# Kernel optimization log

Measured on AMD Instinct MI355X. Metric: run time of the kernel, lower is better.

## Reference

```python
import jax, jax.numpy as jnp
import numpy as np

N_NODES = 50000
N_EDGES = 300000
NODE_DIM = 11
EDGE_DIM = 5
HID = 256
L = 4
G = 1024  # num graphs
BN_EPS = 1e-5


def setup_inputs() -> dict:
    key = jax.random.key(0)
    ks = jax.random.split(key, 24)
    s = 0.05
    inp = {
        "x": jax.random.normal(ks[0], (N_NODES, NODE_DIM), jnp.float32),
        "edge_index": jax.random.randint(ks[1], (2, N_EDGES), 0, N_NODES, jnp.int32),
        "edge_attr": jax.random.normal(ks[2], (N_EDGES, EDGE_DIM), jnp.float32),
        "batch": jnp.sort(jax.random.randint(ks[3], (N_NODES,), 0, G, jnp.int32)),
        # node encoder
        "enc_W": jax.random.normal(ks[4], (NODE_DIM, HID), jnp.float32) * s,
        "enc_b": jnp.zeros((HID,), jnp.float32),
        # per-layer GINE params (stacked over layers)
        "edge_W": jax.random.normal(ks[5], (L, EDGE_DIM, HID), jnp.float32) * s,
        "edge_b": jnp.zeros((L, HID), jnp.float32),
        "mlp_W1": jax.random.normal(ks[6], (L, HID, HID), jnp.float32) * s,
        "mlp_b1": jnp.zeros((L, HID), jnp.float32),
        "mlp_W2": jax.random.normal(ks[7], (L, HID, HID), jnp.float32) * s,
        "mlp_b2": jnp.zeros((L, HID), jnp.float32),
        "bn_g": jnp.ones((L, HID), jnp.float32),
        "bn_b": jnp.zeros((L, HID), jnp.float32),
        # head: 3*HID -> HID -> HID//2 -> 1
        "head_W1": jax.random.normal(ks[8], (3 * HID, HID), jnp.float32) * s,
        "head_b1": jnp.zeros((HID,), jnp.float32),
        "head_W2": jax.random.normal(ks[9], (HID, HID // 2), jnp.float32) * s,
        "head_b2": jnp.zeros((HID // 2,), jnp.float32),
        "head_W3": jax.random.normal(ks[10], (HID // 2, 1), jnp.float32) * s,
        "head_b3": jnp.zeros((1,), jnp.float32),
    }
    return inp


def _forward(x, edge_attr, enc_W, enc_b, edge_W, edge_b, mlp_W1, mlp_b1,
             mlp_W2, mlp_b2, bn_g, bn_b, head_W1, head_b1, head_W2, head_b2,
             head_W3, head_b3, edge_index, batch):
    n = x.shape[0]
    src, dst = edge_index[0], edge_index[1]  # messages flow src(j) -> dst(i)
    h = jax.nn.relu(x @ enc_W + enc_b)  # [N, HID]
    for l in range(L):
        e = edge_attr @ edge_W[l] + edge_b[l]                 # [E, HID]
        msg = jax.nn.relu(h[src] + e)                         # [E, HID]
        aggr = jax.ops.segment_sum(msg, dst, num_segments=n)  # [N, HID]
        z = h + aggr                                          # (1+eps)*h + aggr, eps=0
        z = jax.nn.relu(z @ mlp_W1[l] + mlp_b1[l]) @ mlp_W2[l] + mlp_b2[l]
        # BatchNorm over node dim (batch statistics)
        mu = jnp.mean(z, axis=0)
        var = jnp.var(z, axis=0)
        z = (z - mu) * jax.lax.rsqrt(var + BN_EPS) * bn_g[l] + bn_b[l]
        h = jax.nn.relu(z) + h  # residual
    # mean / add / max pooling per graph
    sums = jax.ops.segment_sum(h, batch, num_segments=G)      # [G, HID]
    cnt = jax.ops.segment_sum(jnp.ones((n, 1), h.dtype), batch, num_segments=G)
    mean = sums / jnp.maximum(cnt, 1.0)
    mx = jax.ops.segment_max(h, batch, num_segments=G)
    g = jnp.concatenate([mean, sums, mx], axis=1)             # [G, 3*HID]
    g = jax.nn.relu(g @ head_W1 + head_b1)
    g = jax.nn.relu(g @ head_W2 + head_b2)
    out = g @ head_W3 + head_b3
    return out.reshape(-1)  # [G]


def reference(x, edge_index, edge_attr, batch, enc_W, enc_b, edge_W, edge_b,
              mlp_W1, mlp_b1, mlp_W2, mlp_b2, bn_g, bn_b, head_W1, head_b1,
              head_W2, head_b2, head_W3, head_b3):
    return _forward(x, edge_attr, enc_W, enc_b, edge_W, edge_b, mlp_W1, mlp_b1,
                    mlp_W2, mlp_b2, bn_g, bn_b, head_W1, head_b1, head_W2,
                    head_b2, head_W3, head_b3, edge_index, batch)
```

## Files before the change

### kernel.cpp

```cpp
#include <hip/hip_runtime.h>

#define N_NODES 50000
#define N_EDGES 300000
#define G_GRAPHS 1024
#define HID 256
#define NLAYERS 4
#define PAD_SLOTS (N_EDGES + 3 * N_NODES + 64)
#define BMT 224

typedef unsigned short ushort_t;
typedef __attribute__((ext_vector_type(8))) short bf16x8;
typedef __attribute__((ext_vector_type(8))) unsigned short u16x8;
typedef __attribute__((ext_vector_type(4))) float f32x4;

__device__ __forceinline__ float bf2f(ushort_t u) {
  unsigned int x = ((unsigned int)u) << 16;
  return __builtin_bit_cast(float, x);
}
__device__ __forceinline__ ushort_t f2bf(float f) {
  unsigned int x = __builtin_bit_cast(unsigned int, f);
  unsigned int lsb = (x >> 16) & 1u;
  x += 0x7fffu + lsb;
  return (ushort_t)(x >> 16);
}

__global__ __launch_bounds__(256) void k_encoder(const float* __restrict__ x,
    const float* __restrict__ W, const float* __restrict__ b,
    ushort_t* __restrict__ h, int n)
{
  int j = threadIdx.x;
  float wcol[11];
#pragma unroll
  for (int k = 0; k < 11; ++k) wcol[k] = W[k * HID + j];
  float bj = b[j];
  __shared__ float xs[8][11];
  int base = blockIdx.x * 8;
  if (j < 88) {
    int r = j / 11, k = j % 11;
    int row = base + r;
    if (row < n) xs[r][k] = x[row * 11 + k];
  }
  __syncthreads();
#pragma unroll
  for (int r = 0; r < 8; ++r) {
    int row = base + r;
    if (row >= n) break;
    float acc = bj;
#pragma unroll
    for (int k = 0; k < 11; ++k) acc += xs[r][k] * wcol[k];
    h[(size_t)row * HID + j] = f2bf(fmaxf(acc, 0.f));
  }
}

__global__ __launch_bounds__(256) void k_hist(const int* __restrict__ dst,
    int* __restrict__ offs, int E)
{
  int e = blockIdx.x * 256 + threadIdx.x;
  if (e < E) atomicAdd(&offs[dst[e]], 1);
}

__global__ __launch_bounds__(1024) void k_scanA(int* __restrict__ offs,
    int* __restrict__ btot, int n)
{
  __shared__ int wsum[16];
  int tid = threadIdx.x, lane = tid & 63, wid = tid >> 6;
  int idx = blockIdx.x * 1024 + tid;
  int cnt = (idx < n) ? offs[idx] : 0;
  int v = (cnt + 3) & ~3;
  int x = v;
#pragma unroll
  for (int off = 1; off < 64; off <<= 1) {
    int t = __shfl_up(x, off);
    if (lane >= off) x += t;
  }
  if (lane == 63) wsum[wid] = x;
  __syncthreads();
  if (wid == 0 && lane < 16) {
    int w = wsum[lane];
#pragma unroll
    for (int off = 1; off < 16; off <<= 1) {
      int t = __shfl_up(w, off);
      if (lane >= off) w += t;
    }
    wsum[lane] = w;
  }
  __syncthreads();
  int wbase = (wid == 0) ? 0 : wsum[wid - 1];
  if (idx < n) offs[idx] = wbase + x - v;
  if (tid == 0) btot[blockIdx.x] = wsum[15];
}

__global__ __launch_bounds__(1024) void k_scanC(int* __restrict__ offs,
    int* __restrict__ pstart, const int* __restrict__ btot, int n)
{
  __shared__ int sbase;
  if (threadIdx.x == 0) {
    int s = 0;
    for (int i = 0; i < (int)blockIdx.x; ++i) s += btot[i];
    sbase = s;
    if (blockIdx.x == gridDim.x - 1) pstart[n] = s + btot[blockIdx.x];
  }
  __syncthreads();
  int idx = blockIdx.x * 1024 + threadIdx.x;
  if (idx < n) {
    int v = offs[idx] + sbase;
    offs[idx] = v;
    pstart[idx] = v;
  }
}

__global__ __launch_bounds__(256) void k_fill(const int* __restrict__ src,
    const int* __restrict__ dst, int* __restrict__ offs,
    int* __restrict__ esrc, ushort_t* __restrict__ eab,
    const float* __restrict__ ea, int E)
{
  int e = blockIdx.x * 256 + threadIdx.x;
  if (e < E) {
    int d = dst[e];
    int p = atomicAdd(&offs[d], 1);
    esrc[p] = src[e];
    const float* ep = ea + (size_t)e * 5;
    ushort4 lo = make_ushort4(f2bf(ep[0]), f2bf(ep[1]), f2bf(ep[2]), f2bf(ep[3]));
    ushort4 hi = make_ushort4(f2bf(ep[4]), (ushort_t)0x3f80u, 0, 0);
    *(ushort4*)&eab[(size_t)p * 8] = lo;
    *(ushort4*)&eab[(size_t)p * 8 + 4] = hi;
  }
}

__global__ __launch_bounds__(256) void k_prep(const float* __restrict__ W1,
    const float* __restrict__ W2, ushort_t* __restrict__ Wt1,
    ushort_t* __restrict__ Wt2)
{
  __shared__ float ld[16][257];
  int mat = blockIdx.y & (NLAYERS - 1);
  int which = blockIdx.y >> 2;
  const float* Wm = (which ? W2 : W1) + (size_t)mat * HID * HID;
  ushort_t* Wtm = (which ? Wt2 : Wt1) + (size_t)mat * HID * HID;
  int k0 = blockIdx.x * 16;
  int tid = threadIdx.x;
#pragma unroll
  for (int i = 0; i < 16; ++i) ld[i][tid] = Wm[(size_t)(k0 + i) * HID + tid];
  __syncthreads();
#pragma unroll
  for (int v = 0; v < 4; ++v) {
    ushort4 u = make_ushort4(f2bf(ld[v*4+0][tid]), f2bf(ld[v*4+1][tid]),
                             f2bf(ld[v*4+2][tid]), f2bf(ld[v*4+3][tid]));
    *(ushort4*)&Wtm[(size_t)tid * HID + k0 + v * 4] = u;
  }
}

__global__ __launch_bounds__(256) void k_prept(const float* __restrict__ W,
    ushort_t* __restrict__ Wt, int K, int N)
{
  int idx = blockIdx.x * 256 + threadIdx.x;
  if (idx >= K * N) return;
  int n = idx / K, k = idx % K;
  Wt[idx] = f2bf(W[(size_t)k * N + n]);
}

__device__ __forceinline__ void edge_step(bf16x8 ev, ushort4 hv,
    const float4& w0, const float4& w1, const float4& w2, const float4& w3,
    const float4& w4, const float4& bi,
    float& ax, float& ay, float& az, float& aw)
{
  float v0 = bf2f((ushort_t)ev[0]), v1 = bf2f((ushort_t)ev[1]),
        v2 = bf2f((ushort_t)ev[2]), v3 = bf2f((ushort_t)ev[3]),
        v4 = bf2f((ushort_t)ev[4]), fl = bf2f((ushort_t)ev[5]);
  float m0 = bi.x, m1 = bi.y, m2 = bi.z, m3 = bi.w;
  m0 = fmaf(v0, w0.x, m0); m1 = fmaf(v0, w0.y, m1);
  m2 = fmaf(v0, w0.z, m2); m3 = fmaf(v0, w0.w, m3);
  m0 = fmaf(v1, w1.x, m0); m1 = fmaf(v1, w1.y, m1);
  m2 = fmaf(v1, w1.z, m2); m3 = fmaf(v1, w1.w, m3);
  m0 = fmaf(v2, w2.x, m0); m1 = fmaf(v2, w2.y, m1);
  m2 = fmaf(v2, w2.z, m2); m3 = fmaf(v2, w2.w, m3);
  m0 = fmaf(v3, w3.x, m0); m1 = fmaf(v3, w3.y, m1);
  m2 = fmaf(v3, w3.z, m2); m3 = fmaf(v3, w3.w, m3);
  m0 = fmaf(v4, w4.x, m0); m1 = fmaf(v4, w4.y, m1);
  m2 = fmaf(v4, w4.z, m2); m3 = fmaf(v4, w4.w, m3);
  m0 += bf2f(hv.x); m1 += bf2f(hv.y); m2 += bf2f(hv.z); m3 += bf2f(hv.w);
  ax = fmaf(fl, fmaxf(m0, 0.f), ax);
  ay = fmaf(fl, fmaxf(m1, 0.f), ay);
  az = fmaf(fl, fmaxf(m2, 0.f), az);
  aw = fmaf(fl, fmaxf(m3, 0.f), aw);
}

__global__ __launch_bounds__(256) void k_gather(const ushort_t* __restrict__ h,
    const int* __restrict__ pstart, const int* __restrict__ esrc,
    const ushort_t* __restrict__ eab, const float* __restrict__ eW,
    const float* __restrict__ eb, ushort_t* __restrict__ zin,
    float* __restrict__ stats, int n)
{
  int tid = threadIdx.x;
  if (blockIdx.x == 0) { stats[tid] = 0.f; stats[HID + tid] = 0.f; }
  int wave = tid >> 6, lane = tid & 63;
  int c4 = lane * 4;
  float4 w0 = *(const float4*)&eW[0 * HID + c4];
  float4 w1 = *(const float4*)&eW[1 * HID + c4];
  float4 w2 = *(const float4*)&eW[2 * HID + c4];
  float4 w3 = *(const float4*)&eW[3 * HID + c4];
  float4 w4 = *(const float4*)&eW[4 * HID + c4];
  float4 bi = *(const float4*)&eb[c4];
  int n0 = (blockIdx.x * 4 + wave) * 4;
  if (n0 >= n) return;
  int e0 = __builtin_amdgcn_readfirstlane(pstart[n0]);
  int e1 = __builtin_amdgcn_readfirstlane(pstart[n0 + 1]);
  int e2 = __builtin_amdgcn_readfirstlane(pstart[n0 + 2]);
  int e3 = __builtin_amdgcn_readfirstlane(pstart[n0 + 3]);
  int e4 = __builtin_amdgcn_readfirstlane(pstart[n0 + 4]);
  float A[4][4];
#pragma unroll
  for (int j = 0; j < 4; ++j) {
    ushort4 hv = *(const ushort4*)&h[(size_t)(n0 + j) * HID + c4];
    A[j][0] = bf2f(hv.x); A[j][1] = bf2f(hv.y);
    A[j][2] = bf2f(hv.z); A[j][3] = bf2f(hv.w);
  }
  int p = e0, pend = e4;
  if (p < pend) {
    int sA0 = esrc[p],     sA1 = esrc[p + 1], sA2 = esrc[p + 2], sA3 = esrc[p + 3];
    int sB0 = esrc[p + 4], sB1 = esrc[p + 5], sB2 = esrc[p + 6], sB3 = esrc[p + 7];
    bf16x8 eaA0 = *(const bf16x8*)&eab[(size_t)(p + 0) * 8];
    bf16x8 eaA1 = *(const bf16x8*)&eab[(size_t)(p + 1) * 8];
    bf16x8 eaA2 = *(const bf16x8*)&eab[(size_t)(p + 2) * 8];
    bf16x8 eaA3 = *(const bf16x8*)&eab[(size_t)(p + 3) * 8];
    bf16x8 eaB0 = *(const bf16x8*)&eab[(size_t)(p + 4) * 8];
    bf16x8 eaB1 = *(const bf16x8*)&eab[(size_t)(p + 5) * 8];
    bf16x8 eaB2 = *(const bf16x8*)&eab[(size_t)(p + 6) * 8];
    bf16x8 eaB3 = *(const bf16x8*)&eab[(size_t)(p + 7) * 8];
    ushort4 hA0 = *(const ushort4*)&h[(size_t)sA0 * HID + c4];
    ushort4 hA1 = *(const ushort4*)&h[(size_t)sA1 * HID + c4];
    ushort4 hA2 = *(const ushort4*)&h[(size_t)sA2 * HID + c4];
    ushort4 hA3 = *(const ushort4*)&h[(size_t)sA3 * HID + c4];
    ushort4 hB0 = *(const ushort4*)&h[(size_t)sB0 * HID + c4];
    ushort4 hB1 = *(const ushort4*)&h[(size_t)sB1 * HID + c4];
    ushort4 hB2 = *(const ushort4*)&h[(size_t)sB2 * HID + c4];
    ushort4 hB3 = *(const ushort4*)&h[(size_t)sB3 * HID + c4];
    int sC0 = esrc[p + 8],  sC1 = esrc[p + 9],  sC2 = esrc[p + 10], sC3 = esrc[p + 11];
    int sD0 = esrc[p + 12], sD1 = esrc[p + 13], sD2 = esrc[p + 14], sD3 = esrc[p + 15];
    while (true) {
      {
        float c0 = 0.f, c1 = 0.f, c2 = 0.f, c3 = 0.f;
        edge_step(eaA0, hA0, w0, w1, w2, w3, w4, bi, c0, c1, c2, c3);
        edge_step(eaA1, hA1, w0, w1, w2, w3, w4, bi, c0, c1, c2, c3);
        edge_step(eaA2, hA2, w0, w1, w2, w3, w4, bi, c0, c1, c2, c3);
        edge_step(eaA3, hA3, w0, w1, w2, w3, w4, bi, c0, c1, c2, c3);
        if (p < e1)      { A[0][0] += c0; A[0][1] += c1; A[0][2] += c2; A[0][3] += c3; }
        else if (p < e2) { A[1][0] += c0; A[1][1] += c1; A[1][2] += c2; A[1][3] += c3; }
        else if (p < e3) { A[2][0] += c0; A[2][1] += c1; A[2][2] += c2; A[2][3] += c3; }
        else             { A[3][0] += c0; A[3][1] += c1; A[3][2] += c2; A[3][3] += c3; }
      }
      p += 4;
      if (p >= pend) break;
      eaA0 = *(const bf16x8*)&eab[(size_t)(p + 4) * 8];
      eaA1 = *(const bf16x8*)&eab[(size_t)(p + 5) * 8];
      eaA2 = *(const bf16x8*)&eab[(size_t)(p + 6) * 8];
      eaA3 = *(const bf16x8*)&eab[(size_t)(p + 7) * 8];
      hA0 = *(const ushort4*)&h[(size_t)sC0 * HID + c4];
      hA1 = *(const ushort4*)&h[(size_t)sC1 * HID + c4];
      hA2 = *(const ushort4*)&h[(size_t)sC2 * HID + c4];
      hA3 = *(const ushort4*)&h[(size_t)sC3 * HID + c4];
      sC0 = esrc[p + 12]; sC1 = esrc[p + 13]; sC2 = esrc[p + 14]; sC3 = esrc[p + 15];
      {
        float c0 = 0.f, c1 = 0.f, c2 = 0.f, c3 = 0.f;
        edge_step(eaB0, hB0, w0, w1, w2, w3, w4, bi, c0, c1, c2, c3);
        edge_step(eaB1, hB1, w0, w1, w2, w3, w4, bi, c0, c1, c2, c3);
        edge_step(eaB2, hB2, w0, w1, w2, w3, w4, bi, c0, c1, c2, c3);
        edge_step(eaB3, hB3, w0, w1, w2, w3, w4, bi, c0, c1, c2, c3);
        if (p < e1)      { A[0][0] += c0; A[0][1] += c1; A[0][2] += c2; A[0][3] += c3; }
        else if (p < e2) { A[1][0] += c0; A[1][1] += c1; A[1][2] += c2; A[1][3] += c3; }
        else if (p < e3) { A[2][0] += c0; A[2][1] += c1; A[2][2] += c2; A[2][3] += c3; }
        else             { A[3][0] += c0; A[3][1] += c1; A[3][2] += c2; A[3][3] += c3; }
      }
      p += 4;
      if (p >= pend) break;
      eaB0 = *(const bf16x8*)&eab[(size_t)(p + 4) * 8];
      eaB1 = *(const bf16x8*)&eab[(size_t)(p + 5) * 8];
      eaB2 = *(const bf16x8*)&eab[(size_t)(p + 6) * 8];
      eaB3 = *(const bf16x8*)&eab[(size_t)(p + 7) * 8];
      hB0 = *(const ushort4*)&h[(size_t)sD0 * HID + c4];
      hB1 = *(const ushort4*)&h[(size_t)sD1 * HID + c4];
      hB2 = *(const ushort4*)&h[(size_t)sD2 * HID + c4];
      hB3 = *(const ushort4*)&h[(size_t)sD3 * HID + c4];
      sD0 = esrc[p + 12]; sD1 = esrc[p + 13]; sD2 = esrc[p + 14]; sD3 = esrc[p + 15];
    }
  }
#pragma unroll
  for (int j = 0; j < 4; ++j) {
    *(ushort4*)&zin[(size_t)(n0 + j) * HID + c4] =
        make_ushort4(f2bf(A[j][0]), f2bf(A[j][1]), f2bf(A[j][2]), f2bf(A[j][3]));
  }
}

__global__ __launch_bounds__(512, 1) void k_mlp(const ushort_t* __restrict__ A,
    const ushort_t* __restrict__ Wt1, const float* __restrict__ b1,
    const ushort_t* __restrict__ Wt2, const float* __restrict__ b2,
    ushort_t* __restrict__ out, float* __restrict__ stats, int M)
{
  __shared__ alignas(16) ushort_t T[BMT][264];
  int tid = threadIdx.x;
  int wave = tid >> 6, lane = tid & 63;
  int m = lane & 15, quad = lane >> 4;
  int col0 = wave * 32;
  int row0 = blockIdx.x * BMT;

#pragma unroll
  for (int i = 0; i < 14; ++i) {
    int flat = i * 512 + tid;
    int row = flat >> 5, kc = flat & 31;
    int gr = row0 + row; if (gr > M - 1) gr = M - 1;
    u16x8 v = *(const u16x8*)(A + (size_t)gr * HID + kc * 8);
    *(u16x8*)&T[row][kc * 8] = v;
  }
  bf16x8 w1f[2][8];
#pragma unroll
  for (int nt = 0; nt < 2; ++nt)
#pragma unroll
    for (int kt = 0; kt < 8; ++kt)
      w1f[nt][kt] = *(const bf16x8*)(
          Wt1 + (size_t)(col0 + nt * 16 + m) * HID + kt * 32 + quad * 8);
  float bv1[2] = {b1[col0 + m], b1[col0 + 16 + m]};
  float bv2[2] = {b2[col0 + m], b2[col0 + 16 + m]};
  __syncthreads();

  f32x4 acc[14][2];
#pragma unroll
  for (int mt = 0; mt < 14; ++mt) {
    acc[mt][0] = (f32x4){0.f, 0.f, 0.f, 0.f};
    acc[mt][1] = (f32x4){0.f, 0.f, 0.f, 0.f};
    bf16x8 af[8];
#pragma unroll
    for (int kt = 0; kt < 8; ++kt)
      af[kt] = *(const bf16x8*)&T[mt * 16 + m][kt * 32 + quad * 8];
#pragma unroll
    for (int kt = 0; kt < 8; ++kt) {
      acc[mt][0] = __builtin_amdgcn_mfma_f32_16x16x32_bf16(af[kt], w1f[0][kt], acc[mt][0], 0, 0, 0);
      acc[mt][1] = __builtin_amdgcn_mfma_f32_16x16x32_bf16(af[kt], w1f[1][kt], acc[mt][1], 0, 0, 0);
    }
  }
  __syncthreads();

#pragma unroll
  for (int mt = 0; mt < 14; ++mt)
#pragma unroll
    for (int nt = 0; nt < 2; ++nt)
#pragma unroll
      for (int reg = 0; reg < 4; ++reg)
        T[mt * 16 + quad * 4 + reg][col0 + nt * 16 + m] =
            f2bf(fmaxf(acc[mt][nt][reg] + bv1[nt], 0.f));
  bf16x8 w2f[2][8];
#pragma unroll
  for (int nt = 0; nt < 2; ++nt)
#pragma unroll
    for (int kt = 0; kt < 8; ++kt)
      w2f[nt][kt] = *(const bf16x8*)(
          Wt2 + (size_t)(col0 + nt * 16 + m) * HID + kt * 32 + quad * 8);
  __syncthreads();

#pragma unroll
  for (int mt = 0; mt < 14; ++mt) {
    acc[mt][0] = (f32x4){0.f, 0.f, 0.f, 0.f};
    acc[mt][1] = (f32x4){0.f, 0.f, 0.f, 0.f};
    bf16x8 af[8];
#pragma unroll
    for (int kt = 0; kt < 8; ++kt)
      af[kt] = *(const bf16x8*)&T[mt * 16 + m][kt * 32 + quad * 8];
#pragma unroll
    for (int kt = 0; kt < 8; ++kt) {
      acc[mt][0] = __builtin_amdgcn_mfma_f32_16x16x32_bf16(af[kt], w2f[0][kt], acc[mt][0], 0, 0, 0);
      acc[mt][1] = __builtin_amdgcn_mfma_f32_16x16x32_bf16(af[kt], w2f[1][kt], acc[mt][1], 0, 0, 0);
    }
  }

  float csum[2] = {0.f, 0.f}, csq[2] = {0.f, 0.f};
#pragma unroll
  for (int mt = 0; mt < 14; ++mt) {
    if (row0 + mt * 16 < M) {
#pragma unroll
      for (int nt = 0; nt < 2; ++nt) {
#pragma unroll
        for (int reg = 0; reg < 4; ++reg) {
          float o = acc[mt][nt][reg] + bv2[nt];
          out[(size_t)(row0 + mt * 16 + quad * 4 + reg) * HID + col0 + nt * 16 + m] = f2bf(o);
          csum[nt] += o; csq[nt] = fmaf(o, o, csq[nt]);
        }
      }
    }
  }
#pragma unroll
  for (int nt = 0; nt < 2; ++nt) {
    float s = csum[nt], q = csq[nt];
    s += __shfl_xor(s, 16); s += __shfl_xor(s, 32);
    q += __shfl_xor(q, 16); q += __shfl_xor(q, 32);
    if (quad == 0) {
      unsafeAtomicAdd(&stats[col0 + nt * 16 + m], s);
      unsafeAtomicAdd(&stats[HID + col0 + nt * 16 + m], q);
    }
  }
}

__global__ __launch_bounds__(256) void k_bn_apply(const ushort_t* __restrict__ z,
    const float* __restrict__ stats, const float* __restrict__ g,
    const float* __restrict__ b, ushort_t* __restrict__ h, int total4)
{
  int idx = blockIdx.x * 256 + threadIdx.x;
  if (idx >= total4) return;
  int col = (idx & 63) * 4;
  const float inv_n = 1.f / (float)N_NODES;
  float sc[4], sh[4];
#pragma unroll
  for (int c = 0; c < 4; ++c) {
    float mu = stats[col + c] * inv_n;
    float var = stats[HID + col + c] * inv_n - mu * mu;
    float rs = rsqrtf(var + 1e-5f);
    sc[c] = g[col + c] * rs;
    sh[c] = b[col + c] - mu * sc[c];
  }
  ushort4 zv = *(const ushort4*)(z + (size_t)idx * 4);
  ushort4 hv = *(const ushort4*)(h + (size_t)idx * 4);
  float o0 = fmaxf(fmaf(bf2f(zv.x), sc[0], sh[0]), 0.f) + bf2f(hv.x);
  float o1 = fmaxf(fmaf(bf2f(zv.y), sc[1], sh[1]), 0.f) + bf2f(hv.y);
  float o2 = fmaxf(fmaf(bf2f(zv.z), sc[2], sh[2]), 0.f) + bf2f(hv.z);
  float o3 = fmaxf(fmaf(bf2f(zv.w), sc[3], sh[3]), 0.f) + bf2f(hv.w);
  *(ushort4*)(h + (size_t)idx * 4) = make_ushort4(f2bf(o0), f2bf(o1), f2bf(o2), f2bf(o3));
}

__device__ __forceinline__ int lbound(const int* __restrict__ b, int n, int key) {
  int lo = 0, hi = n;
  while (lo < hi) {
    int mid = (lo + hi) >> 1;
    if (b[mid] < key) lo = mid + 1; else hi = mid;
  }
  return lo;
}

__global__ __launch_bounds__(256) void k_pool_bn(const ushort_t* __restrict__ z,
    const float* __restrict__ stats, const float* __restrict__ g_,
    const float* __restrict__ b_, const ushort_t* __restrict__ h,
    const int* __restrict__ batch, ushort_t* __restrict__ gf)
{
  int g = blockIdx.x, j = threadIdx.x;
  const float inv_n = 1.f / (float)N_NODES;
  float mu = stats[j] * inv_n;
  float var = stats[HID + j] * inv_n - mu * mu;
  float rs = rsqrtf(var + 1e-5f);
  float sc = g_[j] * rs;
  float sh = b_[j] - mu * sc;
  int lo = lbound(batch, N_NODES, g);
  int hi = lbound(batch, N_NODES, g + 1);
  float s = 0.f, mx = 0.f;
  for (int i = lo; i < hi; ++i) {
    float zv = bf2f(z[(size_t)i * HID + j]);
    float hv = bf2f(h[(size_t)i * HID + j]);
    float v = fmaxf(fmaf(zv, sc, sh), 0.f) + hv;
    s += v; mx = fmaxf(mx, v);
  }
  float cntv = fmaxf((float)(hi - lo), 1.f);
  size_t base = (size_t)g * 768;
  gf[base + j] = f2bf(s / cntv);
  gf[base + 256 + j] = f2bf(s);
  gf[base + 512 + j] = f2bf(mx);
}

template<int KT, int DO_RELU>
__global__ __launch_bounds__(256, 1) void k_head_gemm(const ushort_t* __restrict__ A,
    const ushort_t* __restrict__ Bt, const float* __restrict__ bias,
    ushort_t* __restrict__ out, int M, int N)
{
  const int K = KT * 32;
  int tid = threadIdx.x;
  int wave = tid >> 6, lane = tid & 63;
  int m = lane & 15, quad = lane >> 4;
  int col = (blockIdx.y * 4 + wave) * 16 + m;
  bf16x8 bfrag[KT];
#pragma unroll
  for (int kt = 0; kt < KT; ++kt)
    bfrag[kt] = *(const bf16x8*)(Bt + (size_t)col * K + kt * 32 + quad * 8);
  float bv = bias[col];
  int ntiles = M >> 4;
  for (int t = blockIdx.x; t < ntiles; t += gridDim.x) {
    const ushort_t* Ap = A + (size_t)(t * 16 + m) * K + quad * 8;
    bf16x8 af[KT];
#pragma unroll
    for (int kt = 0; kt < KT; ++kt) af[kt] = *(const bf16x8*)(Ap + kt * 32);
    f32x4 acc = (f32x4){0.f, 0.f, 0.f, 0.f};
#pragma unroll
    for (int kt = 0; kt < KT; ++kt)
      acc = __builtin_amdgcn_mfma_f32_16x16x32_bf16(af[kt], bfrag[kt], acc, 0, 0, 0);
    int rb = t * 16 + quad * 4;
#pragma unroll
    for (int reg = 0; reg < 4; ++reg) {
      float o = acc[reg] + bv;
      if (DO_RELU) o = fmaxf(o, 0.f);
      out[(size_t)(rb + reg) * N + col] = f2bf(o);
    }
  }
}

__global__ __launch_bounds__(256) void k_head_out(const ushort_t* __restrict__ g2,
    const float* __restrict__ W3, const float* __restrict__ b3,
    float* __restrict__ out)
{
  int wave = threadIdx.x >> 6, lane = threadIdx.x & 63;
  int g = blockIdx.x * 4 + wave;
  ushort2 v = *(const ushort2*)&g2[(size_t)g * 128 + lane * 2];
  float p = bf2f(v.x) * W3[lane * 2] + bf2f(v.y) * W3[lane * 2 + 1];
#pragma unroll
  for (int off = 32; off > 0; off >>= 1) p += __shfl_down(p, off);
  if (lane == 0) out[g] = p + b3[0];
}

extern "C" void kernel_launch(void* const* d_in, const int* in_sizes, int n_in,
                              void* d_out, int out_size, void* d_ws, size_t ws_size,
                              hipStream_t stream)
{
  const float* x     = (const float*)d_in[0];
  const int*   ei    = (const int*)d_in[1];
  const float* ea    = (const float*)d_in[2];
  const int*   batch = (const int*)d_in[3];
  const float* encW  = (const float*)d_in[4];
  const float* encB  = (const float*)d_in[5];
  const float* edgeW = (const float*)d_in[6];
  const float* edgeB = (const float*)d_in[7];
  const float* W1    = (const float*)d_in[8];
  const float* b1    = (const float*)d_in[9];
  const float* W2    = (const float*)d_in[10];
  const float* b2    = (const float*)d_in[11];
  const float* bng   = (const float*)d_in[12];
  const float* bnb   = (const float*)d_in[13];
  const float* hW1   = (const float*)d_in[14];
  const float* hb1   = (const float*)d_in[15];
  const float* hW2   = (const float*)d_in[16];
  const float* hb2   = (const float*)d_in[17];
  const float* hW3   = (const float*)d_in[18];
  const float* hb3   = (const float*)d_in[19];
  float* out = (float*)d_out;

  const size_t NH = (size_t)N_NODES * HID;
  char* base = (char*)d_ws;
  auto alloc = [&](size_t bytes) -> char* {
    char* p = base; base += (bytes + 63) & ~(size_t)63; return p;
  };
  float*    stats = (float*)alloc(512 * 4);
  int*      offs  = (int*)alloc(50001 * 4);
  int*      pstart= (int*)alloc(50001 * 4);
  int*      btot  = (int*)alloc(64 * 4);
  int*      esrc  = (int*)alloc((size_t)PAD_SLOTS * 4);
  ushort_t* eab   = (ushort_t*)alloc((size_t)PAD_SLOTS * 8 * 2);
  ushort_t* Wt1   = (ushort_t*)alloc((size_t)NLAYERS * HID * HID * 2);
  ushort_t* Wt2   = (ushort_t*)alloc((size_t)NLAYERS * HID * HID * 2);
  ushort_t* hW1t  = (ushort_t*)alloc((size_t)768 * 256 * 2);
  ushort_t* hW2t  = (ushort_t*)alloc((size_t)256 * 128 * 2);
  ushort_t* gf    = (ushort_t*)alloc((size_t)G_GRAPHS * 768 * 2);
  ushort_t* g1    = (ushort_t*)alloc((size_t)G_GRAPHS * 256 * 2);
  ushort_t* g2    = (ushort_t*)alloc((size_t)G_GRAPHS * 128 * 2);
  ushort_t* zin   = (ushort_t*)alloc(NH * 2);
  ushort_t* h     = (ushort_t*)alloc(NH * 2);

  const int* src = ei;
  const int* dst = ei + N_EDGES;

  hipMemsetAsync(offs, 0, 50001 * sizeof(int), stream);
  hipMemsetAsync(esrc, 0, (size_t)((char*)(eab + (size_t)PAD_SLOTS * 8) - (char*)esrc), stream);
  k_hist<<<(N_EDGES + 255) / 256, 256, 0, stream>>>(dst, offs, N_EDGES);
  const int NSB = (N_NODES + 1023) / 1024;
  k_scanA<<<NSB, 1024, 0, stream>>>(offs, btot, N_NODES);
  k_scanC<<<NSB, 1024, 0, stream>>>(offs, pstart, btot, N_NODES);
  k_fill<<<(N_EDGES + 255) / 256, 256, 0, stream>>>(src, dst, offs, esrc, eab, ea, N_EDGES);
  k_prep<<<dim3(16, 2 * NLAYERS), 256, 0, stream>>>(W1, W2, Wt1, Wt2);
  k_prept<<<(768 * 256 + 255) / 256, 256, 0, stream>>>(hW1, hW1t, 768, 256);
  k_prept<<<(256 * 128 + 255) / 256, 256, 0, stream>>>(hW2, hW2t, 256, 128);

  k_encoder<<<(N_NODES + 7) / 8, 256, 0, stream>>>(x, encW, encB, h, N_NODES);

  const int NB_MLP = (N_NODES + BMT - 1) / BMT;

  for (int l = 0; l < NLAYERS; ++l) {
    k_gather<<<(N_NODES + 15) / 16, 256, 0, stream>>>(
        h, pstart, esrc, eab, edgeW + (size_t)l * 5 * HID, edgeB + (size_t)l * HID,
        zin, stats, N_NODES);
    k_mlp<<<NB_MLP, 512, 0, stream>>>(
        zin, Wt1 + (size_t)l * HID * HID, b1 + (size_t)l * HID,
        Wt2 + (size_t)l * HID * HID, b2 + (size_t)l * HID, zin, stats, N_NODES);
    if (l < NLAYERS - 1) {
      k_bn_apply<<<(N_NODES * HID / 4 + 255) / 256, 256, 0, stream>>>(
          zin, stats, bng + (size_t)l * HID, bnb + (size_t)l * HID, h,
          N_NODES * HID / 4);
    }
  }

  k_pool_bn<<<G_GRAPHS, 256, 0, stream>>>(
      zin, stats, bng + (size_t)(NLAYERS - 1) * HID,
      bnb + (size_t)(NLAYERS - 1) * HID, h, batch, gf);
  k_head_gemm<24, 1><<<dim3(16, 4), 256, 0, stream>>>(gf, hW1t, hb1, g1, G_GRAPHS, 256);
  k_head_gemm<8, 1><<<dim3(16, 2), 256, 0, stream>>>(g1, hW2t, hb2, g2, G_GRAPHS, 128);
  k_head_out<<<G_GRAPHS / 4, 256, 0, stream>>>(g2, hW3, hb3, out);
}
```

Baseline: 537.1 us.

## Fuse BatchNorm apply into MLP kernel via grid-wide barrier

For the first three layers, the MLP kernel no longer writes its pre-norm output. It waits at a spin-based grid barrier until every block has added its column statistics, then applies BatchNorm, ReLU and the residual add straight from the accumulator registers into h. This removes the separate bn_apply launch and the bf16 round trip of z through memory. It relies on all 224 blocks being co-resident (launch_bounds 512,1 on a GPU with enough CUs); otherwise the barrier deadlocks. The spin wait also adds synchronisation cost.

```diff
diff --git a/kernel.cpp b/kernel.cpp
--- a/kernel.cpp
+++ b/kernel.cpp
@@ -290,10 +290,13 @@
   }
 }
 
+template<int FUSE>
 __global__ __launch_bounds__(512, 1) void k_mlp(const ushort_t* __restrict__ A,
     const ushort_t* __restrict__ Wt1, const float* __restrict__ b1,
     const ushort_t* __restrict__ Wt2, const float* __restrict__ b2,
-    ushort_t* __restrict__ out, float* __restrict__ stats, int M)
+    ushort_t* __restrict__ out, float* __restrict__ stats, int M,
+    const float* __restrict__ bng, const float* __restrict__ bnb,
+    ushort_t* __restrict__ hbuf, int* __restrict__ bar)
 {
   __shared__ alignas(16) ushort_t T[BMT][264];
   int tid = threadIdx.x;
@@ -379,7 +382,8 @@
 #pragma unroll
         for (int reg = 0; reg < 4; ++reg) {
           float o = acc[mt][nt][reg] + bv2[nt];
-          out[(size_t)(row0 + mt * 16 + quad * 4 + reg) * HID + col0 + nt * 16 + m] = f2bf(o);
+          if (!FUSE)
+            out[(size_t)(row0 + mt * 16 + quad * 4 + reg) * HID + col0 + nt * 16 + m] = f2bf(o);
           csum[nt] += o; csq[nt] = fmaf(o, o, csq[nt]);
         }
       }
@@ -395,32 +399,45 @@
       unsafeAtomicAdd(&stats[HID + col0 + nt * 16 + m], q);
     }
   }
-}
-
-__global__ __launch_bounds__(256) void k_bn_apply(const ushort_t* __restrict__ z,
-    const float* __restrict__ stats, const float* __restrict__ g,
-    const float* __restrict__ b, ushort_t* __restrict__ h, int total4)
-{
-  int idx = blockIdx.x * 256 + threadIdx.x;
-  if (idx >= total4) return;
-  int col = (idx & 63) * 4;
-  const float inv_n = 1.f / (float)N_NODES;
-  float sc[4], sh[4];
-#pragma unroll
-  for (int c = 0; c < 4; ++c) {
-    float mu = stats[col + c] * inv_n;
-    float var = stats[HID + col + c] * inv_n - mu * mu;
-    float rs = rsqrtf(var + 1e-5f);
-    sc[c] = g[col + c] * rs;
-    sh[c] = b[col + c] - mu * sc[c];
-  }
-  ushort4 zv = *(const ushort4*)(z + (size_t)idx * 4);
-  ushort4 hv = *(const ushort4*)(h + (size_t)idx * 4);
-  float o0 = fmaxf(fmaf(bf2f(zv.x), sc[0], sh[0]), 0.f) + bf2f(hv.x);
-  float o1 = fmaxf(fmaf(bf2f(zv.y), sc[1], sh[1]), 0.f) + bf2f(hv.y);
-  float o2 = fmaxf(fmaf(bf2f(zv.z), sc[2], sh[2]), 0.f) + bf2f(hv.z);
-  float o3 = fmaxf(fmaf(bf2f(zv.w), sc[3], sh[3]), 0.f) + bf2f(hv.w);
-  *(ushort4*)(h + (size_t)idx * 4) = make_ushort4(f2bf(o0), f2bf(o1), f2bf(o2), f2bf(o3));
+
+  if (FUSE) {
+    __threadfence();
+    __syncthreads();
+    if (tid == 0) {
+      atomicAdd(bar, 1);
+      while (atomicAdd(bar, 0) < (int)gridDim.x) __builtin_amdgcn_s_sleep(1);
+    }
+    __syncthreads();
+    const float inv_n = 1.f / (float)N_NODES;
+    float sc[2], sh[2];
+#pragma unroll
+    for (int nt = 0; nt < 2; ++nt) {
+      int c = col0 + nt * 16 + m;
+      float S = unsafeAtomicAdd(&stats[c], 0.f);
+      float Q = unsafeAtomicAdd(&stats[HID + c], 0.f);
+      float mu = S * inv_n;
+      float var = Q * inv_n - mu * mu;
+      float rs = rsqrtf(var + 1e-5f);
+      sc[nt] = bng[c] * rs;
+      sh[nt] = bnb[c] - mu * sc[nt];
+    }
+#pragma unroll
+    for (int mt = 0; mt < 14; ++mt) {
+      if (row0 + mt * 16 < M) {
+#pragma unroll
+        for (int nt = 0; nt < 2; ++nt) {
+          int c = col0 + nt * 16 + m;
+#pragma unroll
+          for (int reg = 0; reg < 4; ++reg) {
+            size_t idx = (size_t)(row0 + mt * 16 + quad * 4 + reg) * HID + c;
+            float o = acc[mt][nt][reg] + bv2[nt];
+            float hv = bf2f(hbuf[idx]);
+            hbuf[idx] = f2bf(fmaxf(fmaf(o, sc[nt], sh[nt]), 0.f) + hv);
+          }
+        }
+      }
+    }
+  }
 }
 
 __device__ __forceinline__ int lbound(const int* __restrict__ b, int n, int key) {
@@ -540,6 +557,7 @@
     char* p = base; base += (bytes + 63) & ~(size_t)63; return p;
   };
   float*    stats = (float*)alloc(512 * 4);
+  int*      bar   = (int*)alloc(16 * 4);
   int*      offs  = (int*)alloc(50001 * 4);
   int*      pstart= (int*)alloc(50001 * 4);
   int*      btot  = (int*)alloc(64 * 4);
@@ -558,6 +576,7 @@
   const int* src = ei;
   const int* dst = ei + N_EDGES;
 
+  hipMemsetAsync(bar, 0, 16 * sizeof(int), stream);
   hipMemsetAsync(offs, 0, 50001 * sizeof(int), stream);
   hipMemsetAsync(esrc, 0, (size_t)((char*)(eab + (size_t)PAD_SLOTS * 8) - (char*)esrc), stream);
   k_hist<<<(N_EDGES + 255) / 256, 256, 0, stream>>>(dst, offs, N_EDGES);
@@ -577,13 +596,16 @@
     k_gather<<<(N_NODES + 15) / 16, 256, 0, stream>>>(
         h, pstart, esrc, eab, edgeW + (size_t)l * 5 * HID, edgeB + (size_t)l * HID,
         zin, stats, N_NODES);
-    k_mlp<<<NB_MLP, 512, 0, stream>>>(
-        zin, Wt1 + (size_t)l * HID * HID, b1 + (size_t)l * HID,
-        Wt2 + (size_t)l * HID * HID, b2 + (size_t)l * HID, zin, stats, N_NODES);
     if (l < NLAYERS - 1) {
-      k_bn_apply<<<(N_NODES * HID / 4 + 255) / 256, 256, 0, stream>>>(
-          zin, stats, bng + (size_t)l * HID, bnb + (size_t)l * HID, h,
-          N_NODES * HID / 4);
+      k_mlp<1><<<NB_MLP, 512, 0, stream>>>(
+          zin, Wt1 + (size_t)l * HID * HID, b1 + (size_t)l * HID,
+          Wt2 + (size_t)l * HID * HID, b2 + (size_t)l * HID, nullptr, stats,
+          N_NODES, bng + (size_t)l * HID, bnb + (size_t)l * HID, h, bar + l);
+    } else {
+      k_mlp<0><<<NB_MLP, 512, 0, stream>>>(
+          zin, Wt1 + (size_t)l * HID * HID, b1 + (size_t)l * HID,
+          Wt2 + (size_t)l * HID * HID, b2 + (size_t)l * HID, zin, stats,
+          N_NODES, nullptr, nullptr, nullptr, nullptr);
     }
   }
 
```

Result: slower. 985.5 us (+83.5%).
